# Optimization experiments

Hardware: AMD Instinct MI355X
Metric: run time of the kernel (lower is better)

The kernel has to match this reference:

```python
import jax, jax.numpy as jnp
import numpy as np

N, D, K = 500000, 64, 1024


def setup_inputs() -> dict:
    key = jax.random.key(0)
    kx, kc = jax.random.split(key)
    x = jax.random.normal(kx, (N, D), dtype=jnp.float32)
    centers = jax.random.normal(kc, (K, D), dtype=jnp.float32)
    return {"x": x, "centers": centers}


def reference(x, centers):
    # KMeans.predict: ids = argmin_k cdist(x, centers).
    # sqrt is monotone, so argmin over squared distances is identical, and the
    # This avoids the N x K x D expansion; the N x K score matrix is the
    # memory-bound hot path a fused kernel would stream over.
    m2 = jnp.sum(centers * centers, axis=-1)          # [K]
    scores = m2[None, :] - 2.0 * (x @ centers.T)      # [N, K]
    ids = jnp.argmin(scores, axis=-1)                 # [N]
    return ids
```

## Files before the change

kernel.cpp:

```cpp
#include <hip/hip_runtime.h>
#include <hip/hip_bf16.h>


#define N_PTS 500000
#define DIM   64
#define K_CENT 1024
#define MARGIN 1.5e-3f

typedef _Float16 half8 __attribute__((ext_vector_type(8)));
typedef float    floatx4 __attribute__((ext_vector_type(4)));

__device__ __forceinline__ float sel4f(int r, float a, float b, float c, float d) {
    return r == 0 ? a : (r == 1 ? b : (r == 2 ? c : d));
}
__device__ __forceinline__ int sel4i(int r, int a, int b, int c, int d) {
    return r == 0 ? a : (r == 1 ? b : (r == 2 ? c : d));
}

__launch_bounds__(1024, 4)
__global__ void kmeans_pass1(const float* __restrict__ x,
                             const float* __restrict__ centers,
                             int* __restrict__ out,
                             int* __restrict__ counter,
                             int* __restrict__ ulist,
                             int capacity)
{
    __shared__ __align__(16) _Float16 ldsC[128 * 144];
    __shared__ float negm2[128];

    const int tid  = threadIdx.x;
    const int lane = tid & 63;
    const int wave = tid >> 6;
    const int l15  = lane & 15;
    const int quad = lane >> 4;

    const int baseP = blockIdx.x * 512 + wave * 32;

    half8 ah[2][2], al[2][2];
    #pragma unroll
    for (int mt = 0; mt < 2; ++mt) {
        int p = baseP + mt * 16 + l15;
        if (p > N_PTS - 1) p = N_PTS - 1;
        const float* xr = x + (size_t)p * DIM + quad * 8;
        #pragma unroll
        for (int h = 0; h < 2; ++h) {
            float4 f0 = *(const float4*)(xr + h * 32);
            float4 f1 = *(const float4*)(xr + h * 32 + 4);
            float v[8] = {f0.x, f0.y, f0.z, f0.w, f1.x, f1.y, f1.z, f1.w};
            half8 hi, lo;
            #pragma unroll
            for (int j = 0; j < 8; ++j) {
                _Float16 hj = (_Float16)v[j];
                hi[j] = hj;
                lo[j] = (_Float16)(v[j] - (float)hj);
            }
            ah[mt][h] = hi; al[mt][h] = lo;
        }
    }

    float m1[2][4], m2v[2][4];
    int   ctb[2][4];
    #pragma unroll
    for (int mt = 0; mt < 2; ++mt)
        #pragma unroll
        for (int r = 0; r < 4; ++r) { m1[mt][r] = -1e30f; m2v[mt][r] = -1e30f; ctb[mt][r] = 0; }

    for (int s = 0; s < 8; ++s) {
        __syncthreads();
        {
            const int c = tid >> 3, e = tid & 7;
            const float* src = centers + (size_t)(s * 128 + c) * DIM + e * 8;
            float4 f0 = *(const float4*)(src);
            float4 f1 = *(const float4*)(src + 4);
            float v[8] = {f0.x, f0.y, f0.z, f0.w, f1.x, f1.y, f1.z, f1.w};
            float ss = 0.f;
            half8 hi, lo;
            #pragma unroll
            for (int j = 0; j < 8; ++j) {
                ss = fmaf(v[j], v[j], ss);
                _Float16 hj = (_Float16)v[j];
                hi[j] = hj;
                lo[j] = (_Float16)(v[j] - (float)hj);
            }
            *(half8*)&ldsC[c * 144 + e * 8]      = hi;
            *(half8*)&ldsC[c * 144 + 72 + e * 8] = lo;
            ss += __shfl_xor(ss, 1);
            ss += __shfl_xor(ss, 2);
            ss += __shfl_xor(ss, 4);
            if (e == 0) negm2[c] = -0.5f * ss;
        }
        __syncthreads();

        #pragma unroll 2
        for (int ctl = 0; ctl < 8; ++ctl) {
            const float ic = negm2[ctl * 16 + l15];
            const _Float16* bp = &ldsC[(ctl * 16 + l15) * 144 + quad * 8];
            half8 bh0 = *(const half8*)bp;
            half8 bh1 = *(const half8*)(bp + 32);
            half8 bl0 = *(const half8*)(bp + 72);
            half8 bl1 = *(const half8*)(bp + 104);
            const int ct = s * 8 + ctl;
            #pragma unroll
            for (int mt = 0; mt < 2; ++mt) {
                floatx4 acc = {ic, ic, ic, ic};
                acc = __builtin_amdgcn_mfma_f32_16x16x32_f16(al[mt][0], bh0, acc, 0, 0, 0);
                acc = __builtin_amdgcn_mfma_f32_16x16x32_f16(ah[mt][0], bl0, acc, 0, 0, 0);
                acc = __builtin_amdgcn_mfma_f32_16x16x32_f16(al[mt][1], bh1, acc, 0, 0, 0);
                acc = __builtin_amdgcn_mfma_f32_16x16x32_f16(ah[mt][1], bl1, acc, 0, 0, 0);
                acc = __builtin_amdgcn_mfma_f32_16x16x32_f16(ah[mt][0], bh0, acc, 0, 0, 0);
                acc = __builtin_amdgcn_mfma_f32_16x16x32_f16(ah[mt][1], bh1, acc, 0, 0, 0);
                #pragma unroll
                for (int r = 0; r < 4; ++r) {
                    float sc = acc[r];
                    m2v[mt][r] = fmaxf(m2v[mt][r], fminf(sc, m1[mt][r]));
                    bool gt = sc > m1[mt][r];
                    m1[mt][r] = gt ? sc : m1[mt][r];
                    ctb[mt][r] = gt ? ct : ctb[mt][r];
                }
            }
        }
    }

    #pragma unroll
    for (int mt = 0; mt < 2; ++mt) {
        #pragma unroll
        for (int r = 0; r < 4; ++r) {
            float a1 = m1[mt][r], a2 = m2v[mt][r];
            int   id = ctb[mt][r] * 16 + l15;
            #pragma unroll
            for (int m = 1; m <= 8; m <<= 1) {
                float o1 = __shfl_xor(a1, m);
                float o2 = __shfl_xor(a2, m);
                int  oid = __shfl_xor(id, m);
                a2 = fmaxf(fmaxf(a2, o2), fminf(a1, o1));
                bool take = (o1 > a1) || (o1 == a1 && oid < id);
                a1 = take ? o1 : a1;
                id = take ? oid : id;
            }
            m1[mt][r] = a1; m2v[mt][r] = a2; ctb[mt][r] = id;
        }
        if (l15 < 4) {
            const int r = l15;
            const int p = baseP + mt * 16 + quad * 4 + r;
            if (p < N_PTS) {
                float a1 = sel4f(r, m1[mt][0], m1[mt][1], m1[mt][2], m1[mt][3]);
                float a2 = sel4f(r, m2v[mt][0], m2v[mt][1], m2v[mt][2], m2v[mt][3]);
                int   id = sel4i(r, ctb[mt][0], ctb[mt][1], ctb[mt][2], ctb[mt][3]);
                out[p] = id;
                if (a1 - a2 < MARGIN) {
                    int slot = atomicAdd(counter, 1);
                    if (slot < capacity) ulist[slot] = p;
                }
            }
        }
    }
}

__launch_bounds__(256)
__global__ void kmeans_pass2(const float* __restrict__ x,
                             const float* __restrict__ centers,
                             int* __restrict__ out,
                             const int* __restrict__ counter,
                             const int* __restrict__ ulist,
                             int capacity)
{
    __shared__ float xs[64];
    __shared__ double wv[4];
    __shared__ int    wi[4];

    int count = *counter;
    if (count > capacity) count = capacity;
    const int tid  = threadIdx.x;
    const int lane = tid & 63;
    const int wave = tid >> 6;

    for (int u = blockIdx.x; u < count; u += gridDim.x) {
        __syncthreads();
        const int p = ulist[u];
        if (tid < 16)
            ((float4*)xs)[tid] = ((const float4*)(x + (size_t)p * DIM))[tid];
        __syncthreads();

        double bv = 1.0e300; int bi = 0;
        #pragma unroll
        for (int j = 0; j < 4; ++j) {
            const int c = tid + j * 256;
            const float4* crow = (const float4*)(centers + (size_t)c * DIM);
            double m2 = 0.0, dot = 0.0;
            #pragma unroll
            for (int kc = 0; kc < 16; ++kc) {
                float4 cv = crow[kc];
                float4 xv = *(const float4*)&xs[kc * 4];
                double c0 = cv.x, c1 = cv.y, c2 = cv.z, c3 = cv.w;
                m2 += c0 * c0 + c1 * c1 + c2 * c2 + c3 * c3;
                dot += c0 * (double)xv.x + c1 * (double)xv.y
                     + c2 * (double)xv.z + c3 * (double)xv.w;
            }
            double s = m2 - 2.0 * dot;
            if (s < bv || (s == bv && c < bi)) { bv = s; bi = c; }
        }
        #pragma unroll
        for (int m = 1; m <= 32; m <<= 1) {
            double ov = __shfl_xor(bv, m);
            int    oi = __shfl_xor(bi, m);
            if (ov < bv || (ov == bv && oi < bi)) { bv = ov; bi = oi; }
        }
        if (lane == 0) { wv[wave] = bv; wi[wave] = bi; }
        __syncthreads();
        if (tid == 0) {
            double v = wv[0]; int i = wi[0];
            #pragma unroll
            for (int w = 1; w < 4; ++w) {
                if (wv[w] < v || (wv[w] == v && wi[w] < i)) { v = wv[w]; i = wi[w]; }
            }
            out[p] = i;
        }
    }
}

extern "C" void kernel_launch(void* const* d_in, const int* in_sizes, int n_in,
                              void* d_out, int out_size, void* d_ws, size_t ws_size,
                              hipStream_t stream)
{
    const float* x       = (const float*)d_in[0];
    const float* centers = (const float*)d_in[1];
    int* out     = (int*)d_out;
    int* counter = (int*)d_ws;
    int* ulist   = (int*)((char*)d_ws + 64);
    int capacity = (int)((ws_size > 64 ? ws_size - 64 : 0) / sizeof(int));
    if (capacity > N_PTS) capacity = N_PTS;

    hipMemsetAsync(d_ws, 0, 64, stream);
    dim3 g1((N_PTS + 511) / 512);
    kmeans_pass1<<<g1, 1024, 0, stream>>>(x, centers, out, counter, ulist, capacity);
    kmeans_pass2<<<512, 256, 0, stream>>>(x, centers, out, counter, ulist, capacity);
}
```

Before: 440.5 us.

## Switch pass1 to 32x32 MFMA with fp16 centers and packed-index argmax

Pass 1 now computes scores with 32x32x16 MFMAs, with centers as the A operand and points as B. Centers are stored only as fp16 hi parts, and points keep a hi/lo split, so each tile needs 8 MFMAs instead of the 12 a full three-term split would take. The per-tile argmax packs the register index into the low 4 mantissa bits, which enables a branch-free max/second-max tree. To absorb the extra approximation error, the uncertainty margin is widened from 1.5e-3 to 8e-3. This sends more points to the fp64 refinement pass, which now gets more blocks.

```diff
diff --git a/kernel.cpp b/kernel.cpp
--- a/kernel.cpp
+++ b/kernel.cpp
@@ -5,19 +5,12 @@
 #define N_PTS 500000
 #define DIM   64
 #define K_CENT 1024
-#define MARGIN 1.5e-3f
-
-typedef _Float16 half8 __attribute__((ext_vector_type(8)));
-typedef float    floatx4 __attribute__((ext_vector_type(4)));
-
-__device__ __forceinline__ float sel4f(int r, float a, float b, float c, float d) {
-    return r == 0 ? a : (r == 1 ? b : (r == 2 ? c : d));
-}
-__device__ __forceinline__ int sel4i(int r, int a, int b, int c, int d) {
-    return r == 0 ? a : (r == 1 ? b : (r == 2 ? c : d));
-}
-
-__launch_bounds__(1024, 4)
+#define MARGIN 8.0e-3f
+
+typedef _Float16 half8   __attribute__((ext_vector_type(8)));
+typedef float    floatx16 __attribute__((ext_vector_type(16)));
+
+__launch_bounds__(512, 4)
 __global__ void kmeans_pass1(const float* __restrict__ x,
                              const float* __restrict__ centers,
                              int* __restrict__ out,
@@ -25,27 +18,25 @@
                              int* __restrict__ ulist,
                              int capacity)
 {
-    __shared__ __align__(16) _Float16 ldsC[128 * 144];
-    __shared__ float negm2[128];
+    __shared__ __align__(16) _Float16 ldsC[256 * 72];
+    __shared__ float negm2[256];
 
     const int tid  = threadIdx.x;
     const int lane = tid & 63;
     const int wave = tid >> 6;
-    const int l15  = lane & 15;
-    const int quad = lane >> 4;
-
-    const int baseP = blockIdx.x * 512 + wave * 32;
-
-    half8 ah[2][2], al[2][2];
-    #pragma unroll
-    for (int mt = 0; mt < 2; ++mt) {
-        int p = baseP + mt * 16 + l15;
-        if (p > N_PTS - 1) p = N_PTS - 1;
-        const float* xr = x + (size_t)p * DIM + quad * 8;
+    const int col  = lane & 31;
+    const int h    = lane >> 5;
+
+    const int p  = blockIdx.x * 256 + wave * 32 + col;
+    const int pc = p > N_PTS - 1 ? N_PTS - 1 : p;
+
+    half8 bh[4], bl[4];
+    {
+        const float* xr = x + (size_t)pc * DIM + h * 8;
         #pragma unroll
-        for (int h = 0; h < 2; ++h) {
-            float4 f0 = *(const float4*)(xr + h * 32);
-            float4 f1 = *(const float4*)(xr + h * 32 + 4);
+        for (int c = 0; c < 4; ++c) {
+            float4 f0 = *(const float4*)(xr + c * 16);
+            float4 f1 = *(const float4*)(xr + c * 16 + 4);
             float v[8] = {f0.x, f0.y, f0.z, f0.w, f1.x, f1.y, f1.z, f1.w};
             half8 hi, lo;
             #pragma unroll
@@ -54,103 +45,111 @@
                 hi[j] = hj;
                 lo[j] = (_Float16)(v[j] - (float)hj);
             }
-            ah[mt][h] = hi; al[mt][h] = lo;
-        }
-    }
-
-    float m1[2][4], m2v[2][4];
-    int   ctb[2][4];
-    #pragma unroll
-    for (int mt = 0; mt < 2; ++mt)
-        #pragma unroll
-        for (int r = 0; r < 4; ++r) { m1[mt][r] = -1e30f; m2v[mt][r] = -1e30f; ctb[mt][r] = 0; }
-
-    for (int s = 0; s < 8; ++s) {
+            bh[c] = hi; bl[c] = lo;
+        }
+    }
+
+    float m1 = -3.0e38f, m2 = -3.0e38f;
+    int   ctb = 0;
+
+    for (int s = 0; s < 4; ++s) {
         __syncthreads();
         {
-            const int c = tid >> 3, e = tid & 7;
-            const float* src = centers + (size_t)(s * 128 + c) * DIM + e * 8;
-            float4 f0 = *(const float4*)(src);
-            float4 f1 = *(const float4*)(src + 4);
-            float v[8] = {f0.x, f0.y, f0.z, f0.w, f1.x, f1.y, f1.z, f1.w};
+            const int c = tid >> 1, hh = tid & 1;
+            const float* src = centers + (size_t)(s * 256 + c) * DIM + hh * 32;
             float ss = 0.f;
-            half8 hi, lo;
+            #pragma unroll
+            for (int g = 0; g < 4; ++g) {
+                float4 f0 = *(const float4*)(src + g * 8);
+                float4 f1 = *(const float4*)(src + g * 8 + 4);
+                float v[8] = {f0.x, f0.y, f0.z, f0.w, f1.x, f1.y, f1.z, f1.w};
+                half8 hi;
+                #pragma unroll
+                for (int j = 0; j < 8; ++j) {
+                    ss = fmaf(v[j], v[j], ss);
+                    hi[j] = (_Float16)v[j];
+                }
+                *(half8*)&ldsC[c * 72 + hh * 32 + g * 8] = hi;
+            }
+            float oss = __shfl_xor(ss, 1);
+            if (hh == 0) negm2[c] = -0.5f * (ss + oss);
+        }
+        __syncthreads();
+
+        for (int ctl = 0; ctl < 8; ++ctl) {
+            const int ct = s * 8 + ctl;
+            const float* nm = &negm2[ctl * 32 + 4 * h];
+            float4 q0 = *(const float4*)(nm);
+            float4 q1 = *(const float4*)(nm + 8);
+            float4 q2 = *(const float4*)(nm + 16);
+            float4 q3 = *(const float4*)(nm + 24);
+            floatx16 acc;
+            acc[0]=q0.x; acc[1]=q0.y; acc[2]=q0.z; acc[3]=q0.w;
+            acc[4]=q1.x; acc[5]=q1.y; acc[6]=q1.z; acc[7]=q1.w;
+            acc[8]=q2.x; acc[9]=q2.y; acc[10]=q2.z; acc[11]=q2.w;
+            acc[12]=q3.x; acc[13]=q3.y; acc[14]=q3.z; acc[15]=q3.w;
+
+            const _Float16* ap = &ldsC[(ctl * 32 + col) * 72 + h * 8];
+            #pragma unroll
+            for (int c = 0; c < 4; ++c) {
+                half8 a = *(const half8*)(ap + c * 16);
+                acc = __builtin_amdgcn_mfma_f32_32x32x16_f16(a, bh[c], acc, 0, 0, 0);
+                acc = __builtin_amdgcn_mfma_f32_32x32x16_f16(a, bl[c], acc, 0, 0, 0);
+            }
+
+            float kk[16];
+            #pragma unroll
+            for (int i = 0; i < 16; ++i) {
+                unsigned u = (__float_as_uint(acc[i]) & 0xFFFFFFF0u) | (unsigned)i;
+                kk[i] = __uint_as_float(u);
+            }
+            float M8[8], S8[8];
             #pragma unroll
             for (int j = 0; j < 8; ++j) {
-                ss = fmaf(v[j], v[j], ss);
-                _Float16 hj = (_Float16)v[j];
-                hi[j] = hj;
-                lo[j] = (_Float16)(v[j] - (float)hj);
-            }
-            *(half8*)&ldsC[c * 144 + e * 8]      = hi;
-            *(half8*)&ldsC[c * 144 + 72 + e * 8] = lo;
-            ss += __shfl_xor(ss, 1);
-            ss += __shfl_xor(ss, 2);
-            ss += __shfl_xor(ss, 4);
-            if (e == 0) negm2[c] = -0.5f * ss;
-        }
-        __syncthreads();
-
-        #pragma unroll 2
-        for (int ctl = 0; ctl < 8; ++ctl) {
-            const float ic = negm2[ctl * 16 + l15];
-            const _Float16* bp = &ldsC[(ctl * 16 + l15) * 144 + quad * 8];
-            half8 bh0 = *(const half8*)bp;
-            half8 bh1 = *(const half8*)(bp + 32);
-            half8 bl0 = *(const half8*)(bp + 72);
-            half8 bl1 = *(const half8*)(bp + 104);
-            const int ct = s * 8 + ctl;
-            #pragma unroll
-            for (int mt = 0; mt < 2; ++mt) {
-                floatx4 acc = {ic, ic, ic, ic};
-                acc = __builtin_amdgcn_mfma_f32_16x16x32_f16(al[mt][0], bh0, acc, 0, 0, 0);
-                acc = __builtin_amdgcn_mfma_f32_16x16x32_f16(ah[mt][0], bl0, acc, 0, 0, 0);
-                acc = __builtin_amdgcn_mfma_f32_16x16x32_f16(al[mt][1], bh1, acc, 0, 0, 0);
-                acc = __builtin_amdgcn_mfma_f32_16x16x32_f16(ah[mt][1], bl1, acc, 0, 0, 0);
-                acc = __builtin_amdgcn_mfma_f32_16x16x32_f16(ah[mt][0], bh0, acc, 0, 0, 0);
-                acc = __builtin_amdgcn_mfma_f32_16x16x32_f16(ah[mt][1], bh1, acc, 0, 0, 0);
-                #pragma unroll
-                for (int r = 0; r < 4; ++r) {
-                    float sc = acc[r];
-                    m2v[mt][r] = fmaxf(m2v[mt][r], fminf(sc, m1[mt][r]));
-                    bool gt = sc > m1[mt][r];
-                    m1[mt][r] = gt ? sc : m1[mt][r];
-                    ctb[mt][r] = gt ? ct : ctb[mt][r];
-                }
-            }
-        }
-    }
-
-    #pragma unroll
-    for (int mt = 0; mt < 2; ++mt) {
-        #pragma unroll
-        for (int r = 0; r < 4; ++r) {
-            float a1 = m1[mt][r], a2 = m2v[mt][r];
-            int   id = ctb[mt][r] * 16 + l15;
-            #pragma unroll
-            for (int m = 1; m <= 8; m <<= 1) {
-                float o1 = __shfl_xor(a1, m);
-                float o2 = __shfl_xor(a2, m);
-                int  oid = __shfl_xor(id, m);
-                a2 = fmaxf(fmaxf(a2, o2), fminf(a1, o1));
-                bool take = (o1 > a1) || (o1 == a1 && oid < id);
-                a1 = take ? o1 : a1;
-                id = take ? oid : id;
-            }
-            m1[mt][r] = a1; m2v[mt][r] = a2; ctb[mt][r] = id;
-        }
-        if (l15 < 4) {
-            const int r = l15;
-            const int p = baseP + mt * 16 + quad * 4 + r;
-            if (p < N_PTS) {
-                float a1 = sel4f(r, m1[mt][0], m1[mt][1], m1[mt][2], m1[mt][3]);
-                float a2 = sel4f(r, m2v[mt][0], m2v[mt][1], m2v[mt][2], m2v[mt][3]);
-                int   id = sel4i(r, ctb[mt][0], ctb[mt][1], ctb[mt][2], ctb[mt][3]);
-                out[p] = id;
-                if (a1 - a2 < MARGIN) {
-                    int slot = atomicAdd(counter, 1);
-                    if (slot < capacity) ulist[slot] = p;
-                }
+                M8[j] = fmaxf(kk[2*j], kk[2*j+1]);
+                S8[j] = fminf(kk[2*j], kk[2*j+1]);
+            }
+            float M4[4], S4[4];
+            #pragma unroll
+            for (int j = 0; j < 4; ++j) {
+                M4[j] = fmaxf(M8[2*j], M8[2*j+1]);
+                S4[j] = fmaxf(fmaxf(fminf(M8[2*j], M8[2*j+1]), S8[2*j]), S8[2*j+1]);
+            }
+            float M2a[2], S2a[2];
+            #pragma unroll
+            for (int j = 0; j < 2; ++j) {
+                M2a[j] = fmaxf(M4[2*j], M4[2*j+1]);
+                S2a[j] = fmaxf(fmaxf(fminf(M4[2*j], M4[2*j+1]), S4[2*j]), S4[2*j+1]);
+            }
+            float M16 = fmaxf(M2a[0], M2a[1]);
+            float S16 = fmaxf(fmaxf(fminf(M2a[0], M2a[1]), S2a[0]), S2a[1]);
+
+            m2 = fmaxf(fmaxf(m2, S16), fminf(M16, m1));
+            bool gt = M16 > m1;
+            m1 = gt ? M16 : m1;
+            ctb = gt ? ct : ctb;
+        }
+    }
+
+    {
+        unsigned u = __float_as_uint(m1);
+        int reg = (int)(u & 15u);
+        int row = (reg & 3) + 8 * (reg >> 2) + 4 * h;
+        int cid = ctb * 32 + row;
+
+        float o1 = __shfl_xor(m1, 32);
+        float o2 = __shfl_xor(m2, 32);
+        int  ocid = __shfl_xor(cid, 32);
+        float nm2 = fmaxf(fmaxf(m2, o2), fminf(m1, o1));
+        bool take = o1 > m1;
+        float nm1 = take ? o1 : m1;
+        int  ncid = take ? ocid : cid;
+
+        if (h == 0 && p < N_PTS) {
+            out[p] = ncid;
+            if (nm1 - nm2 < MARGIN) {
+                int slot = atomicAdd(counter, 1);
+                if (slot < capacity) ulist[slot] = p;
             }
         }
     }
@@ -186,18 +185,18 @@
         for (int j = 0; j < 4; ++j) {
             const int c = tid + j * 256;
             const float4* crow = (const float4*)(centers + (size_t)c * DIM);
-            double m2 = 0.0, dot = 0.0;
+            double m2s = 0.0, dot = 0.0;
             #pragma unroll
             for (int kc = 0; kc < 16; ++kc) {
                 float4 cv = crow[kc];
                 float4 xv = *(const float4*)&xs[kc * 4];
                 double c0 = cv.x, c1 = cv.y, c2 = cv.z, c3 = cv.w;
-                m2 += c0 * c0 + c1 * c1 + c2 * c2 + c3 * c3;
+                m2s += c0 * c0 + c1 * c1 + c2 * c2 + c3 * c3;
                 dot += c0 * (double)xv.x + c1 * (double)xv.y
                      + c2 * (double)xv.z + c3 * (double)xv.w;
             }
-            double s = m2 - 2.0 * dot;
-            if (s < bv || (s == bv && c < bi)) { bv = s; bi = c; }
+            double sc = m2s - 2.0 * dot;
+            if (sc < bv || (sc == bv && c < bi)) { bv = sc; bi = c; }
         }
         #pragma unroll
         for (int m = 1; m <= 32; m <<= 1) {
@@ -231,7 +230,7 @@
     if (capacity > N_PTS) capacity = N_PTS;
 
     hipMemsetAsync(d_ws, 0, 64, stream);
-    dim3 g1((N_PTS + 511) / 512);
-    kmeans_pass1<<<g1, 1024, 0, stream>>>(x, centers, out, counter, ulist, capacity);
-    kmeans_pass2<<<512, 256, 0, stream>>>(x, centers, out, counter, ulist, capacity);
+    dim3 g1((N_PTS + 255) / 256);
+    kmeans_pass1<<<g1, 512, 0, stream>>>(x, centers, out, counter, ulist, capacity);
+    kmeans_pass2<<<1024, 256, 0, stream>>>(x, centers, out, counter, ulist, capacity);
 }
```

Result: slower. 491.1 us (+11.5%).
